# Performance work log

Hardware: AMD Instinct MI355X
Metric: run time of the kernel (lower is better)

The kernel has to match this reference:

```python
import math
import jax, jax.numpy as jnp
import numpy as np

B, S, D, H, E = 4, 1024, 1024, 16, 8
HD = D // H


def gelu_new(x):
    # BERT/GPT tanh-approx GELU (NewGELUActivation)
    c = math.sqrt(2.0 / math.pi)
    return 0.5 * x * (1.0 + jnp.tanh(c * (x + 0.044715 * x ** 3)))


def setup_inputs() -> dict:
    key = jax.random.key(0)
    ks = jax.random.split(key, 12)
    s = 0.02
    return {
        "x": jax.random.normal(ks[0], (B, S, D), jnp.float32),
        "Wq": jax.random.normal(ks[1], (D, D), jnp.float32) * s,
        "bq": jnp.zeros((D,), jnp.float32),
        "Wk": jax.random.normal(ks[2], (D, D), jnp.float32) * s,
        "bk": jnp.zeros((D,), jnp.float32),
        "Wv": jax.random.normal(ks[3], (D, D), jnp.float32) * s,
        "bv": jnp.zeros((D,), jnp.float32),
        "Wg": jax.random.normal(ks[4], (D, E), jnp.float32) * s,
        "bg": jnp.zeros((E,), jnp.float32),
        "W1": jax.random.normal(ks[5], (E, D, D), jnp.float32) * s,
        "b1": jnp.zeros((E, D), jnp.float32),
        "W2": jax.random.normal(ks[6], (E, D, D), jnp.float32) * s,
        "b2": jnp.zeros((E, D), jnp.float32),
    }


def reference(x, Wq, bq, Wk, bk, Wv, bv, Wg, bg, W1, b1, W2, b2):
    b = x.shape[0]
    # ---- Attention (faithful to original: no head transpose, so attention
    # is computed ACROSS HEADS per token: scores are [B,S,H,H]) ----
    Q = (x @ Wq + bq).reshape(b, -1, H, HD)
    K = (x @ Wk + bk).reshape(b, -1, H, HD)
    V = (x @ Wv + bv).reshape(b, -1, H, HD)
    scores = jnp.einsum('bsqd,bskd->bsqk', Q, K) / (HD ** 0.5)  # [B,S,H,H]
    attn = jax.nn.softmax(scores, axis=-1)
    out = jnp.einsum('bsqk,bskd->bsqd', attn, V)  # [B,S,H,HD]
    # torch: out.transpose(1,2).contiguous().view(B,-1,H*HD)
    a = jnp.transpose(out, (0, 2, 1, 3)).reshape(b, -1, D)  # [B,S,D]

    # ---- ComplexMoE: dense all-experts + sequence-mean gating ----
    gates = jax.nn.softmax(a.mean(axis=1) @ Wg + bg, axis=-1)  # [B,E]
    h = gelu_new(jnp.einsum('bsd,edh->bseh', a, W1) + b1)       # [B,S,E,D]
    eo = jnp.einsum('bseh,ehf->bsef', h, W2) + b2               # [B,S,E,D]
    return jnp.einsum('be,bsed->bsd', gates, eo)                # [B,S,D]
```

## Files before the change

kernel.cpp:

```cpp
#include <hip/hip_runtime.h>
#include <stdint.h>

#define AS1 __attribute__((address_space(1)))
#define AS3 __attribute__((address_space(3)))

typedef short v8s __attribute__((ext_vector_type(8)));
typedef float v4f __attribute__((ext_vector_type(4)));

__device__ __forceinline__ float b2f(unsigned short u) {
  return __uint_as_float(((unsigned int)u) << 16);
}
__device__ __forceinline__ unsigned short f2bu(float f) {
  unsigned int u = __float_as_uint(f);
  u += 0x7fffu + ((u >> 16) & 1u);
  return (unsigned short)(u >> 16);
}

__device__ __forceinline__ void gload16(const void* g, const void* l) {
  __builtin_amdgcn_global_load_lds(
      (const AS1 void*)(uintptr_t)g,
      (AS3 void*)(unsigned)(uintptr_t)l,
      16, 0, 0);
}

#define BAR __builtin_amdgcn_s_barrier()
#define VMC2 asm volatile("s_waitcnt vmcnt(2)" ::: "memory")
#define VMC0 asm volatile("s_waitcnt vmcnt(0)" ::: "memory")

__global__ __launch_bounds__(256)
void transpose_all(const float* __restrict__ wq, const float* __restrict__ wk,
                   const float* __restrict__ wv, const float* __restrict__ w1,
                   const float* __restrict__ w2,
                   unsigned short* __restrict__ Wqt,
                   unsigned short* __restrict__ W1t,
                   unsigned short* __restrict__ W2t)
{
  __shared__ float t[64][65];
  const int z = blockIdx.z;
  const float* src;
  unsigned short* dst;
  int ld;
  if (z < 3) {
    src = (z == 0) ? wq : (z == 1) ? wk : wv;
    dst = Wqt + (long long)z * 1048576;
    ld = 1024;
  } else if (z < 11) {
    src = w1 + (long long)(z - 3) * 1048576;
    dst = W1t + (long long)(z - 3) * 1048576;
    ld = 1024;
  } else {
    src = w2 + (long long)(z - 11) * 1048576;
    dst = W2t + (long long)(z - 11) * 1024;
    ld = 8192;
  }
  const int k0 = blockIdx.y * 64, n0 = blockIdx.x * 64;
  const int tr  = threadIdx.x >> 4;
  const int tc4 = (threadIdx.x & 15) * 4;
#pragma unroll
  for (int p = 0; p < 4; ++p) {
    float4 v = *(const float4*)(src + (long long)(k0 + tr + p * 16) * 1024 + n0 + tc4);
    t[tr + p * 16][tc4 + 0] = v.x;
    t[tr + p * 16][tc4 + 1] = v.y;
    t[tr + p * 16][tc4 + 2] = v.z;
    t[tr + p * 16][tc4 + 3] = v.w;
  }
  __syncthreads();
#pragma unroll
  for (int p = 0; p < 4; ++p) {
    const int n = tr + p * 16;
    ushort4 o;
    o.x = f2bu(t[tc4 + 0][n]);
    o.y = f2bu(t[tc4 + 1][n]);
    o.z = f2bu(t[tc4 + 2][n]);
    o.w = f2bu(t[tc4 + 3][n]);
    *(ushort4*)(dst + (long long)(n0 + n) * ld + k0 + tc4) = o;
  }
}

__global__ __launch_bounds__(256)
void cvt_f32_bf16(const float* __restrict__ src, unsigned short* __restrict__ dst, int n)
{
  const int i = (blockIdx.x * 256 + threadIdx.x) * 4;
  if (i >= n) return;
  float4 v = *(const float4*)(src + i);
  ushort4 o;
  o.x = f2bu(v.x); o.y = f2bu(v.y); o.z = f2bu(v.z); o.w = f2bu(v.w);
  *(ushort4*)(dst + i) = o;
}

template<int MH>
__device__ __forceinline__ void read_a(v8s af[4][2],
    const unsigned short* pa, int wm, int rswz)
{
#pragma unroll
  for (int i = 0; i < 4; ++i)
#pragma unroll
    for (int s = 0; s < 2; ++s)
      af[i][s] = *(const v8s*)(pa + MH*8192 + ((((wm*4 + i)*2 + s) << 9) | rswz));
}

template<int NH>
__device__ __forceinline__ void read_b(v8s bfr[2][2],
    const unsigned short* pb, int wn, int rswz)
{
#pragma unroll
  for (int j = 0; j < 2; ++j)
#pragma unroll
    for (int s = 0; s < 2; ++s)
      bfr[j][s] = *(const v8s*)(pb + NH*8192 + ((((wn*2 + j)*2 + s) << 9) | rswz));
}

template<int MH, int NH>
__device__ __forceinline__ void mfma16(v4f acc[8][4], v8s af[4][2], v8s bfr[2][2])
{
  __builtin_amdgcn_s_setprio(1);
#pragma unroll
  for (int i = 0; i < 4; ++i)
#pragma unroll
    for (int j = 0; j < 2; ++j)
#pragma unroll
      for (int s = 0; s < 2; ++s)
        acc[MH*4+i][NH*2+j] = __builtin_amdgcn_mfma_f32_16x16x32_bf16(
            af[i][s], bfr[j][s], acc[MH*4+i][NH*2+j], 0, 0, 0);
  __builtin_amdgcn_s_setprio(0);
}

#define STAGE(G, LD, LDSBASE, GROW0, KT) do { \
    gload16((G) + (long long)((GROW0) + sRow) * (LD) + (KT) + sCol, \
            (LDSBASE) + w512); \
    gload16((G) + (long long)((GROW0) + 64 + sRow) * (LD) + (KT) + sCol, \
            (LDSBASE) + 4096 + w512); \
  } while (0)

template<int EPI>
__global__ __launch_bounds__(512, 2)
void gemm256(const unsigned short* __restrict__ A, int lda,
             const unsigned short* __restrict__ Bt, int ldb,
             const float* __restrict__ bias,
             void* __restrict__ out0, unsigned short* __restrict__ pbs,
             int kLen, const float* __restrict__ gates)
{
  __shared__ __align__(16) unsigned short lds[65536];
  unsigned short* As0 = lds;
  unsigned short* As1 = lds + 16384;
  unsigned short* Bs0 = lds + 32768;
  unsigned short* Bs1 = lds + 49152;

  const int tid  = threadIdx.x;
  const int lane = tid & 63;
  const int w    = tid >> 6;
  const int wm   = w >> 2;
  const int wn   = w & 3;
  const int m0   = blockIdx.y * 256;
  const int n0   = blockIdx.x * 256;
  const int z    = blockIdx.z;
  const int kBase = (EPI == 3) ? z * kLen : 0;

  const int sRow = (w >> 1) * 16 + (lane >> 2);
  const int sCol = (w & 1) * 32 + (((lane & 3) * 8) ^ (((lane >> 5) & 1) << 4));
  const int rr   = lane & 15;
  const int kgrp = lane >> 4;
  const int rswz = (rr * 32 + kgrp * 8) ^ ((rr & 8) << 1);
  const int w512 = w * 512;

  v4f acc[8][4] = {};
  v8s af[4][2], b0[2][2], b1[2][2];

  const int iters = kLen >> 7;

  STAGE(A,  lda, As0,        m0,       kBase);
  STAGE(A,  lda, As0 + 8192, m0 + 128, kBase);
  STAGE(Bt, ldb, Bs0,        n0,       kBase);
  STAGE(Bt, ldb, Bs0 + 8192, n0 + 128, kBase);
  STAGE(A,  lda, As1,        m0,       kBase + 64);
  VMC2;
  BAR;

  for (int it = 0; it < iters; ++it) {
    const bool nl = (it != iters - 1);
    const int k0t = kBase + it * 128;
    const int kT1 = k0t + 64, kT2 = k0t + 128, kT3 = k0t + 192;

    read_a<0>(af, As0, wm, rswz);
    read_b<0>(b0, Bs0, wn, rswz);
    read_b<1>(b1, Bs0, wn, rswz);
    STAGE(Bt, ldb, Bs1, n0, kT1);
    mfma16<0,0>(acc, af, b0);
    BAR;
    STAGE(Bt, ldb, Bs1 + 8192, n0 + 128, kT1);
    mfma16<0,1>(acc, af, b1);
    BAR;
    read_a<1>(af, As0, wm, rswz);
    STAGE(A, lda, As1 + 8192, m0 + 128, kT1);
    mfma16<1,1>(acc, af, b1);
    BAR;
    if (nl) STAGE(A, lda, As0, m0, kT2);
    mfma16<1,0>(acc, af, b0);
    if (nl) { VMC2; } else { VMC0; }
    BAR;
    read_a<0>(af, As1, wm, rswz);
    read_b<0>(b0, Bs1, wn, rswz);
    read_b<1>(b1, Bs1, wn, rswz);
    if (nl) STAGE(Bt, ldb, Bs0, n0, kT2);
    mfma16<0,0>(acc, af, b0);
    BAR;
    if (nl) STAGE(Bt, ldb, Bs0 + 8192, n0 + 128, kT2);
    mfma16<0,1>(acc, af, b1);
    BAR;
    read_a<1>(af, As1, wm, rswz);
    if (nl) STAGE(A, lda, As0 + 8192, m0 + 128, kT2);
    mfma16<1,1>(acc, af, b1);
    BAR;
    if (nl) STAGE(A, lda, As1, m0, kT3);
    mfma16<1,0>(acc, af, b0);
    if (nl) { VMC2; }
    BAR;
  }

  const int lr4 = (lane >> 4) * 4;
  const int lc  = lane & 15;
  float gate = 0.f;
  if (EPI == 1) gate = gates[(m0 >> 10) * 8 + (n0 >> 10)];

#pragma unroll
  for (int mi = 0; mi < 8; ++mi) {
    const int rowb = m0 + (mi >> 2) * 128 + wm * 64 + (mi & 3) * 16 + lr4;
#pragma unroll
    for (int nj = 0; nj < 4; ++nj) {
      const int col = n0 + (nj >> 1) * 128 + wn * 32 + (nj & 1) * 16 + lc;
#pragma unroll
      for (int r = 0; r < 4; ++r) {
        const int row = rowb + r;
        float v = acc[mi][nj][r];
        if (EPI == 0) {
          v += bias[col];
          const int which = col >> 10;
          ((unsigned short*)out0)[(long long)which * 4194304 + (long long)row * 1024 + (col & 1023)] = f2bu(v);
        } else if (EPI == 1) {
          v += bias[col];
          float u = 0.7978845608028654f * (v + 0.044715f * v * v * v);
          u = fminf(fmaxf(u, -15.f), 15.f);
          float e2 = __expf(2.f * u);
          float th = (e2 - 1.f) / (e2 + 1.f);
          ((unsigned short*)out0)[(long long)row * 8192 + col] = f2bu(gate * 0.5f * v * (1.f + th));
        } else {
          if (z == 0) ((float*)out0)[(long long)row * 1024 + col] = v;
          else pbs[(long long)(z - 1) * 4194304 + (long long)row * 1024 + col] = f2bu(v);
        }
      }
    }
  }
}

__global__ __launch_bounds__(256)
void reduce3(float* __restrict__ out, const unsigned short* __restrict__ pb,
             const float* __restrict__ bias2)
{
  const int i = (blockIdx.x * 256 + threadIdx.x) * 4;
  const int b = i >> 20;
  const int n = i & 1023;
  float4 a = *(const float4*)(out + i);
  ushort4 p0 = *(const ushort4*)(pb + i);
  ushort4 p1 = *(const ushort4*)(pb + 4194304 + i);
  ushort4 p2 = *(const ushort4*)(pb + 8388608 + i);
  float4 bb = *(const float4*)(bias2 + b * 1024 + n);
  a.x += b2f(p0.x) + b2f(p1.x) + b2f(p2.x) + bb.x;
  a.y += b2f(p0.y) + b2f(p1.y) + b2f(p2.y) + bb.y;
  a.z += b2f(p0.z) + b2f(p1.z) + b2f(p2.z) + bb.z;
  a.w += b2f(p0.w) + b2f(p1.w) + b2f(p2.w) + bb.w;
  *(float4*)(out + i) = a;
}

__global__ __launch_bounds__(256)
void attn_kernel(const unsigned short* __restrict__ Qb,
                 const unsigned short* __restrict__ Kb,
                 const unsigned short* __restrict__ Vb,
                 unsigned short* __restrict__ a)
{
  const int token = blockIdx.x;
  const int b = token >> 10, s = token & 1023;
  __shared__ float Qs[16][65], Ks[16][65], Vs[16][65];
  __shared__ float attn_s[16][17];
  const int t = threadIdx.x;
  const long long base = (long long)token * 1024;

  {
    const int i0 = t * 4;
    const int hh = i0 >> 6, dd = i0 & 63;
    ushort4 qv = *(const ushort4*)(Qb + base + i0);
    ushort4 kv = *(const ushort4*)(Kb + base + i0);
    ushort4 vv = *(const ushort4*)(Vb + base + i0);
    Qs[hh][dd+0]=b2f(qv.x); Qs[hh][dd+1]=b2f(qv.y); Qs[hh][dd+2]=b2f(qv.z); Qs[hh][dd+3]=b2f(qv.w);
    Ks[hh][dd+0]=b2f(kv.x); Ks[hh][dd+1]=b2f(kv.y); Ks[hh][dd+2]=b2f(kv.z); Ks[hh][dd+3]=b2f(kv.w);
    Vs[hh][dd+0]=b2f(vv.x); Vs[hh][dd+1]=b2f(vv.y); Vs[hh][dd+2]=b2f(vv.z); Vs[hh][dd+3]=b2f(vv.w);
  }
  __syncthreads();

  const int q = t >> 4, k = t & 15;
  float sc = 0.f;
#pragma unroll
  for (int d = 0; d < 64; ++d) sc += Qs[q][d] * Ks[k][d];
  sc *= 0.125f;
  float mx = sc;
#pragma unroll
  for (int m = 1; m < 16; m <<= 1) mx = fmaxf(mx, __shfl_xor(mx, m, 64));
  float ex = __expf(sc - mx);
  float sum = ex;
#pragma unroll
  for (int m = 1; m < 16; m <<= 1) sum += __shfl_xor(sum, m, 64);
  attn_s[q][k] = ex / sum;
  __syncthreads();

  const int hd = t & 63;
  const int wv = t >> 6;
#pragma unroll
  for (int r = 0; r < 4; ++r) {
    const int qq = wv * 4 + r;
    float o = 0.f;
#pragma unroll
    for (int kk = 0; kk < 16; ++kk) o += attn_s[qq][kk] * Vs[kk][hd];
    a[(long long)b * 1048576 + (long long)(qq * 64 + (s >> 4)) * 1024 + (s & 15) * 64 + hd] = f2bu(o);
  }
}

__global__ __launch_bounds__(256)
void col_sum_part(const unsigned short* __restrict__ a, float* __restrict__ part)
{
  const int b = blockIdx.x;
  const int y = blockIdx.y;
  const int d4 = threadIdx.x * 4;
  const unsigned short* p = a + (long long)b * 1048576 + (long long)y * 131072 + d4;
  float s0 = 0.f, s1 = 0.f, s2 = 0.f, s3 = 0.f;
  for (int i = 0; i < 128; ++i) {
    ushort4 v = *(const ushort4*)(p + i * 1024);
    s0 += b2f(v.x); s1 += b2f(v.y); s2 += b2f(v.z); s3 += b2f(v.w);
  }
  float* o = part + (y * 4 + b) * 1024 + d4;
  o[0] = s0; o[1] = s1; o[2] = s2; o[3] = s3;
}

__global__ __launch_bounds__(256)
void gates_bias2(const float* __restrict__ part,
                 const float* __restrict__ Wg,
                 const float* __restrict__ bg,
                 const float* __restrict__ b2,
                 float* __restrict__ gates,
                 float* __restrict__ bias2)
{
  __shared__ float am[4][1024];
  __shared__ float sg[4][8];
  const int t = threadIdx.x;

  for (int i = t; i < 4096; i += 256) {
    const int b = i >> 10, d = i & 1023;
    float s = 0.f;
#pragma unroll
    for (int y = 0; y < 8; ++y) s += part[(y * 4 + b) * 1024 + d];
    am[b][d] = s * (1.f / 1024.f);
  }
  __syncthreads();

  const int pair = t >> 3, subl = t & 7;
  const int b = pair >> 3, e = pair & 7;
  float s = 0.f;
  for (int d = subl * 128; d < subl * 128 + 128; ++d) s += am[b][d] * Wg[d * 8 + e];
#pragma unroll
  for (int m = 1; m < 8; m <<= 1) s += __shfl_xor(s, m, 64);
  if (subl == 0) sg[b][e] = s + bg[e];
  __syncthreads();

  if (t < 4) {
    float mx = -1e30f;
    for (int ee = 0; ee < 8; ++ee) mx = fmaxf(mx, sg[t][ee]);
    float g[8]; float ssum = 0.f;
    for (int ee = 0; ee < 8; ++ee) { g[ee] = __expf(sg[t][ee] - mx); ssum += g[ee]; }
    for (int ee = 0; ee < 8; ++ee) { sg[t][ee] = g[ee] / ssum; gates[t * 8 + ee] = sg[t][ee]; }
  }
  __syncthreads();

  for (int i = t; i < 4096; i += 256) {
    const int bb = i >> 10, n = i & 1023;
    float ss = 0.f;
#pragma unroll
    for (int ee = 0; ee < 8; ++ee) ss += sg[bb][ee] * b2[ee * 1024 + n];
    bias2[i] = ss;
  }
}

extern "C" void kernel_launch(void* const* d_in, const int* in_sizes, int n_in,
                              void* d_out, int out_size, void* d_ws, size_t ws_size,
                              hipStream_t stream) {
  const float* x  = (const float*)d_in[0];
  const float* Wq = (const float*)d_in[1];
  const float* bq = (const float*)d_in[2];
  const float* Wk = (const float*)d_in[3];
  const float* bk = (const float*)d_in[4];
  const float* Wv = (const float*)d_in[5];
  const float* bv = (const float*)d_in[6];
  const float* Wg = (const float*)d_in[7];
  const float* bg = (const float*)d_in[8];
  const float* W1 = (const float*)d_in[9];
  const float* b1 = (const float*)d_in[10];
  const float* W2 = (const float*)d_in[11];
  const float* b2 = (const float*)d_in[12];
  float* out = (float*)d_out;

  if (ws_size < (size_t)109300000) return;

  char* ws = (char*)d_ws;
  unsigned short* xb   = (unsigned short*)(ws + 0);
  unsigned short* Wqt  = (unsigned short*)(ws + 8388608);
  unsigned short* Qb   = (unsigned short*)(ws + 14680064);
  unsigned short* hs   = (unsigned short*)(ws + 0);
  unsigned short* abuf = (unsigned short*)(ws + 67108864);
  unsigned short* pbs  = (unsigned short*)(ws + 67108864);
  unsigned short* W1t  = (unsigned short*)(ws + 75497472);
  unsigned short* W2t  = (unsigned short*)(ws + 92274688);
  float* part  = (float*)(ws + 109051904);
  float* gates = (float*)(ws + 109051904 + 131072);
  float* bias2 = (float*)(ws + 109051904 + 131072 + 512);
  float* bqkv  = (float*)(ws + 109051904 + 131072 + 512 + 16384);

  dim3 tb(256);

  transpose_all<<<dim3(16,16,19), tb, 0, stream>>>(Wq, Wk, Wv, W1, W2, Wqt, W1t, W2t);
  cvt_f32_bf16<<<4096, tb, 0, stream>>>(x, xb, 4194304);
  hipMemcpyAsync(bqkv,        bq, 4096, hipMemcpyDeviceToDevice, stream);
  hipMemcpyAsync(bqkv + 1024, bk, 4096, hipMemcpyDeviceToDevice, stream);
  hipMemcpyAsync(bqkv + 2048, bv, 4096, hipMemcpyDeviceToDevice, stream);

  gemm256<0><<<dim3(12,16,1), 512, 0, stream>>>(xb, 1024, Wqt, 1024, bqkv,
                                                Qb, nullptr, 1024, nullptr);
  attn_kernel<<<4096, tb, 0, stream>>>(Qb, Qb + 4194304, Qb + 8388608, abuf);
  col_sum_part<<<dim3(4,8), tb, 0, stream>>>(abuf, part);
  gates_bias2<<<1, tb, 0, stream>>>(part, Wg, bg, b2, gates, bias2);
  gemm256<1><<<dim3(32,16,1), 512, 0, stream>>>(abuf, 1024, W1t, 1024, b1,
                                                hs, nullptr, 1024, gates);
  gemm256<3><<<dim3(4,16,4), 512, 0, stream>>>(hs, 8192, W2t, 8192, nullptr,
                                               out, pbs, 2048, nullptr);
  reduce3<<<4096, tb, 0, stream>>>(out, pbs, bias2);
}
```

Baseline: 264.1 us.

## Retile GEMM to 1024-thread blocks with 64x64 per-wave tiles and simpler pipeline

```diff
diff --git a/kernel.cpp b/kernel.cpp
--- a/kernel.cpp
+++ b/kernel.cpp
@@ -24,7 +24,7 @@
 }
 
 #define BAR __builtin_amdgcn_s_barrier()
-#define VMC2 asm volatile("s_waitcnt vmcnt(2)" ::: "memory")
+#define VMC4 asm volatile("s_waitcnt vmcnt(4)" ::: "memory")
 #define VMC0 asm volatile("s_waitcnt vmcnt(0)" ::: "memory")
 
 __global__ __launch_bounds__(256)
@@ -88,52 +88,35 @@
   *(ushort4*)(dst + i) = o;
 }
 
-template<int MH>
-__device__ __forceinline__ void read_a(v8s af[4][2],
-    const unsigned short* pa, int wm, int rswz)
-{
-#pragma unroll
-  for (int i = 0; i < 4; ++i)
-#pragma unroll
-    for (int s = 0; s < 2; ++s)
-      af[i][s] = *(const v8s*)(pa + MH*8192 + ((((wm*4 + i)*2 + s) << 9) | rswz));
-}
-
-template<int NH>
-__device__ __forceinline__ void read_b(v8s bfr[2][2],
-    const unsigned short* pb, int wn, int rswz)
-{
-#pragma unroll
-  for (int j = 0; j < 2; ++j)
-#pragma unroll
-    for (int s = 0; s < 2; ++s)
-      bfr[j][s] = *(const v8s*)(pb + NH*8192 + ((((wn*2 + j)*2 + s) << 9) | rswz));
-}
-
-template<int MH, int NH>
-__device__ __forceinline__ void mfma16(v4f acc[8][4], v8s af[4][2], v8s bfr[2][2])
-{
-  __builtin_amdgcn_s_setprio(1);
-#pragma unroll
-  for (int i = 0; i < 4; ++i)
-#pragma unroll
-    for (int j = 0; j < 2; ++j)
-#pragma unroll
-      for (int s = 0; s < 2; ++s)
-        acc[MH*4+i][NH*2+j] = __builtin_amdgcn_mfma_f32_16x16x32_bf16(
-            af[i][s], bfr[j][s], acc[MH*4+i][NH*2+j], 0, 0, 0);
-  __builtin_amdgcn_s_setprio(0);
-}
-
-#define STAGE(G, LD, LDSBASE, GROW0, KT) do { \
-    gload16((G) + (long long)((GROW0) + sRow) * (LD) + (KT) + sCol, \
-            (LDSBASE) + w512); \
-    gload16((G) + (long long)((GROW0) + 64 + sRow) * (LD) + (KT) + sCol, \
-            (LDSBASE) + 4096 + w512); \
+#define STAGE4(AsX, BsX, KT) do { \
+    gload16(pA  + (KT), (AsX) + w512); \
+    gload16(pA2 + (KT), (AsX) + 8192 + w512); \
+    gload16(pB  + (KT), (BsX) + w512); \
+    gload16(pB2 + (KT), (BsX) + 8192 + w512); \
   } while (0)
 
+#define KTILE(BUFA, BUFB) do { \
+    _Pragma("unroll") \
+    for (int s = 0; s < 2; ++s) { \
+      v8s af[4], bf[4]; \
+      _Pragma("unroll") \
+      for (int i = 0; i < 4; ++i) \
+        af[i] = *(const v8s*)((BUFA) + ahalf + ((((wml*4 + i)*2 + s) << 9) | rswz)); \
+      _Pragma("unroll") \
+      for (int j = 0; j < 4; ++j) \
+        bf[j] = *(const v8s*)((BUFB) + bhalf + ((((wnl*4 + j)*2 + s) << 9) | rswz)); \
+      __builtin_amdgcn_s_setprio(1); \
+      _Pragma("unroll") \
+      for (int i = 0; i < 4; ++i) \
+        _Pragma("unroll") \
+        for (int j = 0; j < 4; ++j) \
+          acc[i][j] = __builtin_amdgcn_mfma_f32_16x16x32_bf16(af[i], bf[j], acc[i][j], 0, 0, 0); \
+      __builtin_amdgcn_s_setprio(0); \
+    } \
+  } while (0)
+
 template<int EPI>
-__global__ __launch_bounds__(512, 2)
+__global__ __launch_bounds__(1024, 4)
 void gemm256(const unsigned short* __restrict__ A, int lda,
              const unsigned short* __restrict__ Bt, int ldb,
              const float* __restrict__ bias,
@@ -151,6 +134,8 @@
   const int w    = tid >> 6;
   const int wm   = w >> 2;
   const int wn   = w & 3;
+  const int wml  = wm & 1;
+  const int wnl  = wn & 1;
   const int m0   = blockIdx.y * 256;
   const int n0   = blockIdx.x * 256;
   const int z    = blockIdx.z;
@@ -162,76 +147,57 @@
   const int kgrp = lane >> 4;
   const int rswz = (rr * 32 + kgrp * 8) ^ ((rr & 8) << 1);
   const int w512 = w * 512;
-
-  v4f acc[8][4] = {};
-  v8s af[4][2], b0[2][2], b1[2][2];
-
-  const int iters = kLen >> 7;
-
-  STAGE(A,  lda, As0,        m0,       kBase);
-  STAGE(A,  lda, As0 + 8192, m0 + 128, kBase);
-  STAGE(Bt, ldb, Bs0,        n0,       kBase);
-  STAGE(Bt, ldb, Bs0 + 8192, n0 + 128, kBase);
-  STAGE(A,  lda, As1,        m0,       kBase + 64);
-  VMC2;
+  const int ahalf = (wm >> 1) * 8192;
+  const int bhalf = (wn >> 1) * 8192;
+
+  const unsigned short* pA  = A  + (long long)(m0 + sRow) * lda + kBase + sCol;
+  const unsigned short* pA2 = pA + (long long)128 * lda;
+  const unsigned short* pB  = Bt + (long long)(n0 + sRow) * ldb + kBase + sCol;
+  const unsigned short* pB2 = pB + (long long)128 * ldb;
+
+  v4f acc[4][4] = {};
+
+  const int npair = kLen >> 7;
+
+  STAGE4(As0, Bs0, 0);
+  STAGE4(As1, Bs1, 64);
+  VMC4;
   BAR;
 
-  for (int it = 0; it < iters; ++it) {
-    const bool nl = (it != iters - 1);
-    const int k0t = kBase + it * 128;
-    const int kT1 = k0t + 64, kT2 = k0t + 128, kT3 = k0t + 192;
-
-    read_a<0>(af, As0, wm, rswz);
-    read_b<0>(b0, Bs0, wn, rswz);
-    read_b<1>(b1, Bs0, wn, rswz);
-    STAGE(Bt, ldb, Bs1, n0, kT1);
-    mfma16<0,0>(acc, af, b0);
+  for (int j = 0; j < npair; ++j) {
+    const bool more = (j + 1 < npair);
+    const int kt2 = (2 * j + 2) * 64;
+    const int kt3 = (2 * j + 3) * 64;
+
+    KTILE(As0, Bs0);
     BAR;
-    STAGE(Bt, ldb, Bs1 + 8192, n0 + 128, kT1);
-    mfma16<0,1>(acc, af, b1);
+    if (more) { STAGE4(As0, Bs0, kt2); VMC4; } else { VMC0; }
     BAR;
-    read_a<1>(af, As0, wm, rswz);
-    STAGE(A, lda, As1 + 8192, m0 + 128, kT1);
-    mfma16<1,1>(acc, af, b1);
-    BAR;
-    if (nl) STAGE(A, lda, As0, m0, kT2);
-    mfma16<1,0>(acc, af, b0);
-    if (nl) { VMC2; } else { VMC0; }
-    BAR;
-    read_a<0>(af, As1, wm, rswz);
-    read_b<0>(b0, Bs1, wn, rswz);
-    read_b<1>(b1, Bs1, wn, rswz);
-    if (nl) STAGE(Bt, ldb, Bs0, n0, kT2);
-    mfma16<0,0>(acc, af, b0);
-    BAR;
-    if (nl) STAGE(Bt, ldb, Bs0 + 8192, n0 + 128, kT2);
-    mfma16<0,1>(acc, af, b1);
-    BAR;
-    read_a<1>(af, As1, wm, rswz);
-    if (nl) STAGE(A, lda, As0 + 8192, m0 + 128, kT2);
-    mfma16<1,1>(acc, af, b1);
-    BAR;
-    if (nl) STAGE(A, lda, As1, m0, kT3);
-    mfma16<1,0>(acc, af, b0);
-    if (nl) { VMC2; }
-    BAR;
+    KTILE(As1, Bs1);
+    if (more) {
+      BAR;
+      STAGE4(As1, Bs1, kt3);
+      VMC4;
+      BAR;
+    }
   }
 
   const int lr4 = (lane >> 4) * 4;
   const int lc  = lane & 15;
+  const int row0 = m0 + wm * 64;
+  const int col0 = n0 + wn * 64;
   float gate = 0.f;
   if (EPI == 1) gate = gates[(m0 >> 10) * 8 + (n0 >> 10)];
 
 #pragma unroll
-  for (int mi = 0; mi < 8; ++mi) {
-    const int rowb = m0 + (mi >> 2) * 128 + wm * 64 + (mi & 3) * 16 + lr4;
-#pragma unroll
-    for (int nj = 0; nj < 4; ++nj) {
-      const int col = n0 + (nj >> 1) * 128 + wn * 32 + (nj & 1) * 16 + lc;
+  for (int i = 0; i < 4; ++i) {
+#pragma unroll
+    for (int j = 0; j < 4; ++j) {
+      const int col = col0 + j * 16 + lc;
 #pragma unroll
       for (int r = 0; r < 4; ++r) {
-        const int row = rowb + r;
-        float v = acc[mi][nj][r];
+        const int row = row0 + i * 16 + lr4 + r;
+        float v = acc[i][j][r];
         if (EPI == 0) {
           v += bias[col];
           const int which = col >> 10;
@@ -429,14 +395,14 @@
   hipMemcpyAsync(bqkv + 1024, bk, 4096, hipMemcpyDeviceToDevice, stream);
   hipMemcpyAsync(bqkv + 2048, bv, 4096, hipMemcpyDeviceToDevice, stream);
 
-  gemm256<0><<<dim3(12,16,1), 512, 0, stream>>>(xb, 1024, Wqt, 1024, bqkv,
-                                                Qb, nullptr, 1024, nullptr);
+  gemm256<0><<<dim3(12,16,1), 1024, 0, stream>>>(xb, 1024, Wqt, 1024, bqkv,
+                                                 Qb, nullptr, 1024, nullptr);
   attn_kernel<<<4096, tb, 0, stream>>>(Qb, Qb + 4194304, Qb + 8388608, abuf);
   col_sum_part<<<dim3(4,8), tb, 0, stream>>>(abuf, part);
   gates_bias2<<<1, tb, 0, stream>>>(part, Wg, bg, b2, gates, bias2);
-  gemm256<1><<<dim3(32,16,1), 512, 0, stream>>>(abuf, 1024, W1t, 1024, b1,
-                                                hs, nullptr, 1024, gates);
-  gemm256<3><<<dim3(4,16,4), 512, 0, stream>>>(hs, 8192, W2t, 8192, nullptr,
-                                               out, pbs, 2048, nullptr);
+  gemm256<1><<<dim3(32,16,1), 1024, 0, stream>>>(abuf, 1024, W1t, 1024, b1,
+                                                 hs, nullptr, 1024, gates);
+  gemm256<3><<<dim3(4,16,4), 1024, 0, stream>>>(hs, 8192, W2t, 8192, nullptr,
+                                                out, pbs, 2048, nullptr);
   reduce3<<<4096, tb, 0, stream>>>(out, pbs, bias2);
 }
```

Measured after the change: 327.2 us. 23.9% more time.
